# Optimization experiments

Hardware: AMD Instinct MI355X
Metric: run time of the kernel (lower is better)

Reference implementation:

```python
import jax, jax.numpy as jnp
import numpy as np

B, U, N, D, O = 64, 8, 2048, 512, 512  # batch, units, neurons, input_dim, output_dim
RES_CONN, IN_CONN, BIAS_P = 0.2, 0.2, 0.5


def setup_inputs() -> dict:
    key = jax.random.key(0)
    ks = jax.random.split(key, 10)
    # Recurrent weights: normal * sparse mask, normalized by ~spectral radius
    Wd = jax.random.normal(ks[0], (U, N, N), dtype=jnp.float32)
    Wmask = (jax.random.uniform(ks[1], (U, N, N)) < RES_CONN).astype(jnp.float32)
    W = Wd * Wmask / jnp.sqrt(RES_CONN * N)  # approx unit spectral radius
    # Input weights: fixed_bernoulli -> {0,1} sparse matrix
    Win = (jax.random.uniform(ks[2], (U, D, N)) < IN_CONN).astype(jnp.float32)
    bias = (jax.random.uniform(ks[3], (U, 1, N)) < BIAS_P).astype(jnp.float32)
    Wout = jax.random.normal(ks[4], (U, N, O), dtype=jnp.float32)
    sr = jax.random.uniform(ks[5], (U, 1, 1), dtype=jnp.float32)
    adaptive_lr = jax.random.uniform(ks[6], (U, D, 1), dtype=jnp.float32)
    temperature = jnp.ones((1,), dtype=jnp.float32)
    X = jax.random.normal(ks[7], (B, U, D), dtype=jnp.float32)
    state = jax.random.normal(ks[8], (B, U, N), dtype=jnp.float32)
    return {"X": X, "state": state, "W": W, "Win": Win, "bias": bias,
            "Wout": Wout, "sr": sr, "adaptive_lr": adaptive_lr,
            "temperature": temperature}


def reference(X, state, W, Win, bias, Wout, sr, adaptive_lr, temperature):
    # X: [B,U,D], state: [B,U,N]
    x = X[:, :, None, :]       # [B,U,1,D]
    s = state[:, :, None, :]   # [B,U,1,N]
    # adaptive learning rate: softmax over units
    logits = jnp.einsum('buid,udk->buik', x, adaptive_lr) / temperature  # [B,U,1,1]
    lr = jax.nn.softmax(logits, axis=1)
    # _sparse_mm_subhead == masked matmul (W's zeros contribute nothing)
    feed = jnp.einsum('bud,udn->bun', X, Win)[:, :, None, :]           # [B,U,1,N]
    echo = jnp.einsum('bun,unm->bum', state, W * sr)[:, :, None, :] + bias
    new_state = (1.0 - lr) * s + lr * jnp.tanh(feed + echo)            # [B,U,1,N]
    output = jnp.einsum('buin,uno->buio', new_state, Wout)             # [B,U,1,O]
    return new_state.squeeze(2), output.squeeze(2)
```

## Files before the change

### kernel.cpp

```cpp
#include <hip/hip_runtime.h>

#define B_ 64
#define U_ 8
#define N_ 2048
#define D_ 512
#define O_ 512
#define NS_ELEMS ((long)B_ * U_ * N_)

typedef __attribute__((ext_vector_type(8))) short short8;
typedef __attribute__((ext_vector_type(8))) float float8;
typedef __attribute__((ext_vector_type(4))) float float4v;
typedef __attribute__((ext_vector_type(4))) unsigned short ushort4v;
typedef __attribute__((ext_vector_type(16))) float floatx16;

__device__ __forceinline__ float bf2f(unsigned short b) {
    unsigned int u = ((unsigned int)b) << 16;
    float f; __builtin_memcpy(&f, &u, 4); return f;
}
__device__ __forceinline__ unsigned short f2bf(float f) {
    unsigned int u; __builtin_memcpy(&u, &f, 4);
    u += 0x7FFFu + ((u >> 16) & 1u);
    return (unsigned short)(u >> 16);
}
__device__ __forceinline__ bool is_bf(const void* temp) {
    return ((const unsigned short*)temp)[0] == 0x3F80u;
}
__device__ __forceinline__ float ldg1(const void* p, long i, bool bf) {
    return bf ? bf2f(((const unsigned short*)p)[i]) : ((const float*)p)[i];
}
__device__ __forceinline__ short8 ld8(const void* p, long i, bool bf) {
    if (bf) return *(const short8*)((const unsigned short*)p + i);
    float8 v = *(const float8*)((const float*)p + i);
    short8 r;
#pragma unroll
    for (int e = 0; e < 8; ++e) r[e] = (short)f2bf(v[e]);
    return r;
}
__device__ __forceinline__ short8 ld8s(const void* p, long i, bool bf, float s) {
    short8 r;
    if (bf) {
        short8 v = *(const short8*)((const unsigned short*)p + i);
#pragma unroll
        for (int e = 0; e < 8; ++e) r[e] = (short)f2bf(bf2f((unsigned short)v[e]) * s);
    } else {
        float8 v = *(const float8*)((const float*)p + i);
#pragma unroll
        for (int e = 0; e < 8; ++e) r[e] = (short)f2bf(v[e] * s);
    }
    return r;
}
__device__ __forceinline__ void stg1(void* p, long i, bool bf, float v) {
    if (bf) ((unsigned short*)p)[i] = f2bf(v); else ((float*)p)[i] = v;
}
__device__ __forceinline__ int swz(int row, int kbyte) {
    return row * 128 + (kbyte ^ ((row & 7) << 4));
}

__device__ __forceinline__ void gl_lds16(const void* g, void* l) {
    __builtin_amdgcn_global_load_lds(
        (const __attribute__((address_space(1))) unsigned int*)g,
        (__attribute__((address_space(3))) unsigned int*)l, 16, 0, 0);
}
#define WAITV(n) asm volatile("s_waitcnt vmcnt(" #n ")" ::: "memory")

template<bool BF, int NCH>
__device__ __forceinline__ void gemm_stream(
        const char* __restrict__ Apan, long arow_b,
        const char* __restrict__ Bpan, long brow_b,
        char* __restrict__ As,
        char* __restrict__ Bs,
        floatx16& acc, int t) {
    const int w = t >> 6, l = t & 63;
    const int mrow = (w >> 1) * 32 + (l & 31);
    const int ncol = (w & 1) * 32 + (l & 31);
    const int BCH = BF ? 8192 : 16384;
    const int a_r = w * 16 + (l >> 3);
    const long a_g = 16 * ((l & 7) ^ (l >> 3));

#define ISSUE(ck)                                                                   \
    {   char* Ad = As + ((ck) % 3) * 8192 + w * 2048;                               \
        const char* Ag0 = Apan + (long)(ck) * 128;                                  \
        gl_lds16(Ag0 + (long)a_r * arow_b + a_g, Ad);                               \
        gl_lds16(Ag0 + (long)(a_r + 8) * arow_b + a_g, Ad + 1024);                  \
        char* Bd = Bs + ((ck) % 3) * BCH;                                           \
        if (BF) {                                                                   \
            const char* Bg0 = Bpan +                                                \
                (long)((ck) * 64 + w * 16 + (l >> 3)) * brow_b + (l & 7) * 16;      \
            gl_lds16(Bg0, Bd + w * 2048);                                           \
            gl_lds16(Bg0 + 8 * brow_b, Bd + w * 2048 + 1024);                       \
        } else {                                                                    \
            const char* Bg0 = Bpan +                                                \
                (long)((ck) * 64 + w * 16 + (l >> 4)) * brow_b + (l & 15) * 16;     \
            gl_lds16(Bg0, Bd + w * 4096);                                           \
            gl_lds16(Bg0 + 4 * brow_b, Bd + w * 4096 + 1024);                       \
            gl_lds16(Bg0 + 8 * brow_b, Bd + w * 4096 + 2048);                       \
            gl_lds16(Bg0 + 12 * brow_b, Bd + w * 4096 + 3072);                      \
        } }

    ISSUE(0);
    ISSUE(1);
#pragma unroll
    for (int ck = 0; ck < NCH; ++ck) {
        if (ck + 2 < NCH) ISSUE(ck + 2);
        __builtin_amdgcn_sched_barrier(0);
        const int rem = NCH - 1 - ck;
        if (BF) { if (rem >= 2) WAITV(8); else if (rem == 1) WAITV(4); else WAITV(0); }
        else    { if (rem >= 2) WAITV(12); else if (rem == 1) WAITV(6); else WAITV(0); }
        __builtin_amdgcn_s_barrier();
        __builtin_amdgcn_sched_barrier(0);
        const char* Ac = As + (ck % 3) * 8192;
        const char* Bc = Bs + (ck % 3) * BCH;
#pragma unroll
        for (int ks = 0; ks < 4; ++ks) {
            int g = 2 * ks + (l >> 5);
            short8 a = *(const short8*)(Ac + swz(mrow, g * 16));
            short8 bfr;
            if (BF) {
#pragma unroll
                for (int e = 0; e < 8; ++e)
                    bfr[e] = *(const short*)(Bc + (g * 8 + e) * 128 + ncol * 2);
            } else {
#pragma unroll
                for (int e = 0; e < 8; ++e)
                    bfr[e] = (short)f2bf(*(const float*)(Bc + (g * 8 + e) * 256 + ncol * 4));
            }
            acc = __builtin_amdgcn_mfma_f32_32x32x16_bf16(a, bfr, acc, 0, 0, 0);
        }
        __builtin_amdgcn_sched_barrier(0);
        __builtin_amdgcn_s_barrier();
    }
#undef ISSUE
}

__global__ __launch_bounds__(256) void k0_pack(
        const void* __restrict__ state, const void* __restrict__ X,
        const void* __restrict__ sr, const void* __restrict__ temp,
        unsigned short* __restrict__ stC, unsigned short* __restrict__ xC) {
    const bool bf = is_bf(temp);
    const long i = ((long)blockIdx.x * 256 + threadIdx.x) * 4;
    ushort4v o;
    if (i < NS_ELEMS) {
        const int u = (int)(i >> 17), b = (int)((i >> 11) & 63), k = (int)(i & 2047);
        const float srv = ldg1(sr, u, bf);
#pragma unroll
        for (int e = 0; e < 4; ++e)
            o[e] = f2bf(ldg1(state, (long)(b * 8 + u) * 2048 + k + e, bf) * srv);
        *(ushort4v*)(stC + i) = o;
    } else {
        const long j = i - NS_ELEMS;
        const int u = (int)(j >> 15), b = (int)((j >> 9) & 63), k = (int)(j & 511);
#pragma unroll
        for (int e = 0; e < 4; ++e)
            o[e] = f2bf(ldg1(X, (long)(b * 8 + u) * 512 + k + e, bf));
        *(ushort4v*)(xC + j) = o;
    }
}

__global__ __launch_bounds__(512) void k1_lr(
        const void* __restrict__ X, const void* __restrict__ alr,
        const void* __restrict__ temp, float* __restrict__ lrbuf) {
    const bool bf = is_bf(temp);
    const int b = blockIdx.x;
    const int t = threadIdx.x;
    const int u = t >> 6, ln = t & 63;
    float s = 0.f;
#pragma unroll
    for (int e = 0; e < 8; ++e) {
        int d = ln * 8 + e;
        s += ldg1(X, (long)(b * 8 + u) * 512 + d, bf) * ldg1(alr, u * 512 + d, bf);
    }
#pragma unroll
    for (int off = 1; off < 64; off <<= 1) s += __shfl_xor(s, off);
    __shared__ float lg[U_];
    const float T = ldg1(temp, 0, bf);
    if (ln == 0) lg[u] = s / T;
    __syncthreads();
    if (t < U_) {
        float m = lg[0];
#pragma unroll
        for (int i = 1; i < U_; ++i) m = fmaxf(m, lg[i]);
        float den = 0.f;
#pragma unroll
        for (int i = 0; i < U_; ++i) den += expf(lg[i] - m);
        lrbuf[b * U_ + t] = expf(lg[t] - m) / den;
    }
}

template<bool BF>
__device__ __forceinline__ void k2s_body(
        const unsigned short* stC, const unsigned short* xC,
        const void* W, const void* Win, float* slabs,
        char* As, char* Bs, int bid, int t) {
    const int seg = bid >> 8;
    const int u   = (bid >> 5) & 7;
    const int n0  = (bid & 31) * 64;
    const int w = t >> 6, l = t & 63;
    const long esz = BF ? 2 : 4;
    floatx16 acc;
#pragma unroll
    for (int i = 0; i < 16; ++i) acc[i] = 0.f;

    if (seg == 0) {
        gemm_stream<BF, 8>((const char*)xC + (long)u * 65536, 1024,
                           (const char*)Win + ((long)u * D_ * N_ + n0) * esz, N_ * esz,
                           As, Bs, acc, t);
    } else {
        gemm_stream<BF, 8>((const char*)stC + (long)u * 262144 + (long)(seg - 1) * 1024, 4096,
                           (const char*)W + ((long)u * N_ * N_ + (long)(seg - 1) * 512 * N_ + n0) * esz,
                           N_ * esz, As, Bs, acc, t);
    }
    float* slab = slabs + (long)seg * NS_ELEMS;
    const int n = n0 + (w & 1) * 32 + (l & 31);
    const int rowbase = (w >> 1) * 32 + 4 * (l >> 5);
#pragma unroll
    for (int r = 0; r < 16; ++r) {
        int b = rowbase + (r & 3) + 8 * (r >> 2);
        slab[(long)b * (U_ * N_) + u * N_ + n] = acc[r];
    }
}

__global__ __launch_bounds__(256) void k2_stream(
        const unsigned short* __restrict__ stC, const unsigned short* __restrict__ xC,
        const void* __restrict__ W, const void* __restrict__ Win,
        const void* __restrict__ temp, float* __restrict__ slabs) {
    __shared__ alignas(16) char As[3 * 8192];
    __shared__ alignas(16) char Bs[3 * 16384];
    if (is_bf(temp))
        k2s_body<true >(stC, xC, W, Win, slabs, As, Bs, blockIdx.x, threadIdx.x);
    else
        k2s_body<false>(stC, xC, W, Win, slabs, As, Bs, blockIdx.x, threadIdx.x);
}

__global__ void k2b_mix(const float* __restrict__ slabs, const void* __restrict__ state,
                        const void* __restrict__ bias, const void* __restrict__ temp,
                        const float* __restrict__ lrbuf, void* __restrict__ ns,
                        unsigned short* __restrict__ nsC) {
    const bool bf = is_bf(temp);
    const long i = ((long)blockIdx.x * 256 + threadIdx.x) * 4;
    const int b = (int)(i >> 14);
    const int un = (int)(i & 16383);
    const int u = un >> 11, n = un & 2047;
    float4v s = *(const float4v*)(slabs + i);
#pragma unroll
    for (int seg = 1; seg < 5; ++seg) {
        float4v v = *(const float4v*)(slabs + (long)seg * NS_ELEMS + i);
#pragma unroll
        for (int e = 0; e < 4; ++e) s[e] += v[e];
    }
    const float lr = lrbuf[b * U_ + u];
    ushort4v oc;
#pragma unroll
    for (int e = 0; e < 4; ++e) {
        float st = ldg1(state, i + e, bf);
        float bv = ldg1(bias, u * N_ + n + e, bf);
        float v = (1.f - lr) * st + lr * tanhf(s[e] + bv);
        stg1(ns, i + e, bf, v);
        oc[e] = f2bf(v);
    }
    *(ushort4v*)(nsC + ((long)u * 64 + b) * 2048 + n) = oc;
}

template<bool BF>
__device__ __forceinline__ void k3s_body(
        const unsigned short* nsC, const void* Wout, float* part,
        char* As, char* Bs, int bid, int t) {
    const int kc = bid >> 6;
    const int u  = (bid >> 3) & 7;
    const int ot = bid & 7;
    const int o0 = ot * 64;
    const int w = t >> 6, l = t & 63;
    const long esz = BF ? 2 : 4;
    floatx16 acc;
#pragma unroll
    for (int i = 0; i < 16; ++i) acc[i] = 0.f;
    gemm_stream<BF, 4>((const char*)nsC + (long)u * 262144 + (long)kc * 512, 4096,
                       (const char*)Wout + ((long)u * N_ * O_ + (long)kc * 256 * O_ + o0) * esz,
                       O_ * esz, As, Bs, acc, t);
    float* slab = part + (((kc * 8 + u) * 8 + ot) << 12);
    const int oo = (w & 1) * 32 + (l & 31);
    const int rowbase = (w >> 1) * 32 + 4 * (l >> 5);
#pragma unroll
    for (int r = 0; r < 16; ++r) {
        int b = rowbase + (r & 3) + 8 * (r >> 2);
        slab[b * 64 + oo] = acc[r];
    }
}

__global__ __launch_bounds__(256) void k3_stream(
        const unsigned short* __restrict__ nsC, const void* __restrict__ Wout,
        const void* __restrict__ temp, float* __restrict__ part) {
    __shared__ alignas(16) char As[3 * 8192];
    __shared__ alignas(16) char Bs[3 * 16384];
    if (is_bf(temp))
        k3s_body<true >(nsC, Wout, part, As, Bs, blockIdx.x, threadIdx.x);
    else
        k3s_body<false>(nsC, Wout, part, As, Bs, blockIdx.x, threadIdx.x);
}

__global__ void k3_reduce(const float* __restrict__ part, const void* __restrict__ temp,
                          void* __restrict__ outfull, int kcs) {
    const bool bf = is_bf(temp);
    int i = blockIdx.x * 256 + threadIdx.x;
    int b = i >> 12;
    int u = (i >> 9) & 7;
    int o = i & 511;
    int ot = o >> 6, oo = o & 63;
    float s = 0.f;
    for (int kc = 0; kc < kcs; ++kc)
        s += part[(((kc * 8 + u) * 8 + ot) << 12) + b * 64 + oo];
    stg1(outfull, NS_ELEMS + i, bf, s);
}

__global__ __launch_bounds__(256) void k2_state(
        const void* __restrict__ X, const void* __restrict__ state,
        const void* __restrict__ W, const void* __restrict__ Win,
        const void* __restrict__ bias, const void* __restrict__ sr,
        const void* __restrict__ temp, const float* __restrict__ lrbuf,
        void* __restrict__ ns) {
    const bool bf = is_bf(temp);
    const int u  = blockIdx.x >> 5;
    const int n0 = (blockIdx.x & 31) * 64;
    const int t = threadIdx.x;
    const int w = t >> 6, l = t & 63;
    __shared__ alignas(16) char As[8192];
    __shared__ alignas(16) char Bs[8192];
    const float srv = ldg1(sr, u, bf);
    floatx16 acc;
#pragma unroll
    for (int i = 0; i < 16; ++i) acc[i] = 0.f;
    for (int ck = 0; ck < 40; ++ck) {
        const bool feed = ck < 8;
        const void* Ag; long aoff; int lda; float ascale;
        const void* Bg; long boff;
        if (feed) {
            Ag = X;   aoff = (long)u * D_ + ck * 64;          lda = U_ * D_; ascale = 1.f;
            Bg = Win; boff = (long)u * D_ * N_ + (long)(ck * 64) * N_ + n0;
        } else {
            Ag = state; aoff = (long)u * N_ + (ck - 8) * 64;  lda = U_ * N_; ascale = srv;
            Bg = W;     boff = (long)u * N_ * N_ + (long)((ck - 8) * 64) * N_ + n0;
        }
        __syncthreads();
#pragma unroll
        for (int j = 0; j < 2; ++j) {
            int idx = j * 256 + t;
            int row = idx >> 3, cch = idx & 7;
            short8 v = ld8s(Ag, aoff + (long)row * lda + cch * 8, bf, ascale);
            *(short8*)(As + swz(row, cch * 16)) = v;
        }
#pragma unroll
        for (int j = 0; j < 2; ++j) {
            int k = t & 63;
            int c = (t >> 6) + 4 * j;
            short8 v = ld8(Bg, boff + (long)k * N_ + c * 8, bf);
#pragma unroll
            for (int e = 0; e < 8; ++e) {
                int n = c * 8 + e;
                *(unsigned short*)(Bs + swz(n, 2 * k)) = (unsigned short)v[e];
            }
        }
        __syncthreads();
        const int mrow = (w >> 1) * 32 + (l & 31);
        const int ncol = (w & 1) * 32 + (l & 31);
#pragma unroll
        for (int ks = 0; ks < 4; ++ks) {
            int g = 2 * ks + (l >> 5);
            short8 a = *(const short8*)(As + swz(mrow, g * 16));
            short8 b = *(const short8*)(Bs + swz(ncol, g * 16));
            acc = __builtin_amdgcn_mfma_f32_32x32x16_bf16(a, b, acc, 0, 0, 0);
        }
    }
    const int n = n0 + (w & 1) * 32 + (l & 31);
    const int rowbase = (w >> 1) * 32 + 4 * (l >> 5);
    const float biasv = ldg1(bias, u * N_ + n, bf);
#pragma unroll
    for (int r = 0; r < 16; ++r) {
        int b = rowbase + (r & 3) + 8 * (r >> 2);
        float lr = lrbuf[b * U_ + u];
        float st = ldg1(state, (long)b * U_ * N_ + u * N_ + n, bf);
        float v = (1.f - lr) * st + lr * tanhf(acc[r] + biasv);
        stg1(ns, (long)b * U_ * N_ + u * N_ + n, bf, v);
    }
}

__global__ __launch_bounds__(256) void k3_mono(
        const void* __restrict__ ns, const void* __restrict__ Wout,
        const void* __restrict__ temp, void* __restrict__ outfull) {
    const bool bf = is_bf(temp);
    const int u  = (blockIdx.x >> 3) & 7;
    const int ot = blockIdx.x & 7;
    const int o0 = ot * 64;
    const int t = threadIdx.x;
    const int w = t >> 6, l = t & 63;
    __shared__ alignas(16) char As[8192];
    __shared__ alignas(16) char Bs[8192];
    floatx16 acc;
#pragma unroll
    for (int i = 0; i < 16; ++i) acc[i] = 0.f;
    for (int ck = 0; ck < 32; ++ck) {
        const long ka = (long)(ck * 64);
        __syncthreads();
#pragma unroll
        for (int j = 0; j < 2; ++j) {
            int idx = j * 256 + t;
            int row = idx >> 3, cch = idx & 7;
            short8 v = ld8(ns, (long)row * (U_ * N_) + u * N_ + ka + cch * 8, bf);
            *(short8*)(As + swz(row, cch * 16)) = v;
        }
#pragma unroll
        for (int j = 0; j < 2; ++j) {
            int k = t & 63;
            int c = (t >> 6) + 4 * j;
            short8 v = ld8(Wout, (long)u * N_ * O_ + (ka + k) * O_ + o0 + c * 8, bf);
#pragma unroll
            for (int e = 0; e < 8; ++e) {
                int n = c * 8 + e;
                *(unsigned short*)(Bs + swz(n, 2 * k)) = (unsigned short)v[e];
            }
        }
        __syncthreads();
        const int mrow = (w >> 1) * 32 + (l & 31);
        const int ncol = (w & 1) * 32 + (l & 31);
#pragma unroll
        for (int ks = 0; ks < 4; ++ks) {
            int g = 2 * ks + (l >> 5);
            short8 a = *(const short8*)(As + swz(mrow, g * 16));
            short8 b = *(const short8*)(Bs + swz(ncol, g * 16));
            acc = __builtin_amdgcn_mfma_f32_32x32x16_bf16(a, b, acc, 0, 0, 0);
        }
    }
    const int oo = (w & 1) * 32 + (l & 31);
    const int rowbase = (w >> 1) * 32 + 4 * (l >> 5);
#pragma unroll
    for (int r = 0; r < 16; ++r) {
        int b = rowbase + (r & 3) + 8 * (r >> 2);
        stg1(outfull, NS_ELEMS + (long)b * U_ * O_ + u * O_ + o0 + oo, bf, acc[r]);
    }
}

extern "C" void kernel_launch(void* const* d_in, const int* in_sizes, int n_in,
                              void* d_out, int out_size, void* d_ws, size_t ws_size,
                              hipStream_t stream) {
    const void* X     = d_in[0];
    const void* state = d_in[1];
    const void* W     = d_in[2];
    const void* Win   = d_in[3];
    const void* bias  = d_in[4];
    const void* Wout  = d_in[5];
    const void* sr    = d_in[6];
    const void* alr   = d_in[7];
    const void* temp  = d_in[8];

    char* base = (char*)d_ws;
    float* lrbuf        = (float*)base;
    unsigned short* stC = (unsigned short*)(base + 4096);
    unsigned short* xC  = (unsigned short*)(base + 4096 + (2u << 20));
    unsigned short* nsC = (unsigned short*)(base + 4096 + (2u << 20) + (512u << 10));
    float* slabs        = (float*)(base + (8u << 20));
    const size_t need = (8u << 20) + 5 * (size_t)NS_ELEMS * 4;

    k1_lr<<<B_, 512, 0, stream>>>(X, alr, temp, lrbuf);

    if (ws_size >= need) {
        k0_pack  <<<1280, 256, 0, stream>>>(state, X, sr, temp, stC, xC);
        k2_stream<<<1280, 256, 0, stream>>>(stC, xC, W, Win, temp, slabs);
        k2b_mix  <<<NS_ELEMS / 1024, 256, 0, stream>>>(slabs, state, bias, temp, lrbuf, d_out, nsC);
        k3_stream<<<512, 256, 0, stream>>>(nsC, Wout, temp, slabs);
        k3_reduce<<<(B_ * U_ * O_) / 256, 256, 0, stream>>>(slabs, temp, d_out, 8);
    } else {
        k2_state<<<256, 256, 0, stream>>>(X, state, W, Win, bias, sr, temp, lrbuf, d_out);
        k3_mono <<<64, 256, 0, stream>>>(d_out, Wout, temp, d_out);
    }
}
```

Baseline: 70.47 us.

## Rebalance split-K into 3 bf16 slabs and remap block order per XCD

```diff
diff --git a/kernel.cpp b/kernel.cpp
--- a/kernel.cpp
+++ b/kernel.cpp
@@ -6,6 +6,7 @@
 #define D_ 512
 #define O_ 512
 #define NS_ELEMS ((long)B_ * U_ * N_)
+#define OUT_ELEMS ((long)B_ * U_ * O_)
 
 typedef __attribute__((ext_vector_type(8))) short short8;
 typedef __attribute__((ext_vector_type(8))) float float8;
@@ -189,7 +190,7 @@
 template<bool BF>
 __device__ __forceinline__ void k2s_body(
         const unsigned short* stC, const unsigned short* xC,
-        const void* W, const void* Win, float* slabs,
+        const void* W, const void* Win, unsigned short* slabs,
         char* As, char* Bs, int bid, int t) {
     const int seg = bid >> 8;
     const int u   = (bid >> 5) & 7;
@@ -200,38 +201,46 @@
 #pragma unroll
     for (int i = 0; i < 16; ++i) acc[i] = 0.f;
 
+    const char* stP = (const char*)stC + (long)u * 262144;
+    const char* Wp  = (const char*)W + ((long)u * N_ * N_ + n0) * esz;
+
     if (seg == 0) {
         gemm_stream<BF, 8>((const char*)xC + (long)u * 65536, 1024,
                            (const char*)Win + ((long)u * D_ * N_ + n0) * esz, N_ * esz,
                            As, Bs, acc, t);
+        gemm_stream<BF, 8>(stP, 4096, Wp, N_ * esz, As, Bs, acc, t);
+    } else if (seg == 1) {
+        gemm_stream<BF, 12>(stP + 1024, 4096, Wp + (long)512 * N_ * esz, N_ * esz,
+                            As, Bs, acc, t);
     } else {
-        gemm_stream<BF, 8>((const char*)stC + (long)u * 262144 + (long)(seg - 1) * 1024, 4096,
-                           (const char*)W + ((long)u * N_ * N_ + (long)(seg - 1) * 512 * N_ + n0) * esz,
-                           N_ * esz, As, Bs, acc, t);
-    }
-    float* slab = slabs + (long)seg * NS_ELEMS;
+        gemm_stream<BF, 12>(stP + 2560, 4096, Wp + (long)1280 * N_ * esz, N_ * esz,
+                            As, Bs, acc, t);
+    }
+    unsigned short* slab = slabs + (long)seg * NS_ELEMS;
     const int n = n0 + (w & 1) * 32 + (l & 31);
     const int rowbase = (w >> 1) * 32 + 4 * (l >> 5);
 #pragma unroll
     for (int r = 0; r < 16; ++r) {
         int b = rowbase + (r & 3) + 8 * (r >> 2);
-        slab[(long)b * (U_ * N_) + u * N_ + n] = acc[r];
+        slab[(long)b * (U_ * N_) + u * N_ + n] = f2bf(acc[r]);
     }
 }
 
 __global__ __launch_bounds__(256) void k2_stream(
         const unsigned short* __restrict__ stC, const unsigned short* __restrict__ xC,
         const void* __restrict__ W, const void* __restrict__ Win,
-        const void* __restrict__ temp, float* __restrict__ slabs) {
+        const void* __restrict__ temp, unsigned short* __restrict__ slabs) {
     __shared__ alignas(16) char As[3 * 8192];
     __shared__ alignas(16) char Bs[3 * 16384];
+    const int bid = (blockIdx.x % 8) * 96 + blockIdx.x / 8;
     if (is_bf(temp))
-        k2s_body<true >(stC, xC, W, Win, slabs, As, Bs, blockIdx.x, threadIdx.x);
+        k2s_body<true >(stC, xC, W, Win, slabs, As, Bs, bid, threadIdx.x);
     else
-        k2s_body<false>(stC, xC, W, Win, slabs, As, Bs, blockIdx.x, threadIdx.x);
-}
-
-__global__ void k2b_mix(const float* __restrict__ slabs, const void* __restrict__ state,
+        k2s_body<false>(stC, xC, W, Win, slabs, As, Bs, bid, threadIdx.x);
+}
+
+__global__ void k2b_mix(const unsigned short* __restrict__ slabs,
+                        const void* __restrict__ state,
                         const void* __restrict__ bias, const void* __restrict__ temp,
                         const float* __restrict__ lrbuf, void* __restrict__ ns,
                         unsigned short* __restrict__ nsC) {
@@ -240,12 +249,13 @@
     const int b = (int)(i >> 14);
     const int un = (int)(i & 16383);
     const int u = un >> 11, n = un & 2047;
-    float4v s = *(const float4v*)(slabs + i);
-#pragma unroll
-    for (int seg = 1; seg < 5; ++seg) {
-        float4v v = *(const float4v*)(slabs + (long)seg * NS_ELEMS + i);
-#pragma unroll
-        for (int e = 0; e < 4; ++e) s[e] += v[e];
+    float4v s;
+    {
+        ushort4v v0 = *(const ushort4v*)(slabs + i);
+        ushort4v v1 = *(const ushort4v*)(slabs + NS_ELEMS + i);
+        ushort4v v2 = *(const ushort4v*)(slabs + 2 * NS_ELEMS + i);
+#pragma unroll
+        for (int e = 0; e < 4; ++e) s[e] = bf2f(v0[e]) + bf2f(v1[e]) + bf2f(v2[e]);
     }
     const float lr = lrbuf[b * U_ + u];
     ushort4v oc;
@@ -262,7 +272,7 @@
 
 template<bool BF>
 __device__ __forceinline__ void k3s_body(
-        const unsigned short* nsC, const void* Wout, float* part,
+        const unsigned short* nsC, const void* Wout, unsigned short* part,
         char* As, char* Bs, int bid, int t) {
     const int kc = bid >> 6;
     const int u  = (bid >> 3) & 7;
@@ -276,29 +286,31 @@
     gemm_stream<BF, 4>((const char*)nsC + (long)u * 262144 + (long)kc * 512, 4096,
                        (const char*)Wout + ((long)u * N_ * O_ + (long)kc * 256 * O_ + o0) * esz,
                        O_ * esz, As, Bs, acc, t);
-    float* slab = part + (((kc * 8 + u) * 8 + ot) << 12);
+    unsigned short* slab = part + (((kc * 8 + u) * 8 + ot) << 12);
     const int oo = (w & 1) * 32 + (l & 31);
     const int rowbase = (w >> 1) * 32 + 4 * (l >> 5);
 #pragma unroll
     for (int r = 0; r < 16; ++r) {
         int b = rowbase + (r & 3) + 8 * (r >> 2);
-        slab[b * 64 + oo] = acc[r];
+        slab[b * 64 + oo] = f2bf(acc[r]);
     }
 }
 
 __global__ __launch_bounds__(256) void k3_stream(
         const unsigned short* __restrict__ nsC, const void* __restrict__ Wout,
-        const void* __restrict__ temp, float* __restrict__ part) {
+        const void* __restrict__ temp, unsigned short* __restrict__ part) {
     __shared__ alignas(16) char As[3 * 8192];
     __shared__ alignas(16) char Bs[3 * 16384];
+    const int bid = (blockIdx.x % 8) * 64 + blockIdx.x / 8;
     if (is_bf(temp))
-        k3s_body<true >(nsC, Wout, part, As, Bs, blockIdx.x, threadIdx.x);
+        k3s_body<true >(nsC, Wout, part, As, Bs, bid, threadIdx.x);
     else
-        k3s_body<false>(nsC, Wout, part, As, Bs, blockIdx.x, threadIdx.x);
-}
-
-__global__ void k3_reduce(const float* __restrict__ part, const void* __restrict__ temp,
-                          void* __restrict__ outfull, int kcs) {
+        k3s_body<false>(nsC, Wout, part, As, Bs, bid, threadIdx.x);
+}
+
+__global__ void k3_reduce(const unsigned short* __restrict__ part,
+                          const void* __restrict__ temp,
+                          void* __restrict__ outfull) {
     const bool bf = is_bf(temp);
     int i = blockIdx.x * 256 + threadIdx.x;
     int b = i >> 12;
@@ -306,8 +318,9 @@
     int o = i & 511;
     int ot = o >> 6, oo = o & 63;
     float s = 0.f;
-    for (int kc = 0; kc < kcs; ++kc)
-        s += part[(((kc * 8 + u) * 8 + ot) << 12) + b * 64 + oo];
+#pragma unroll
+    for (int kc = 0; kc < 8; ++kc)
+        s += bf2f(part[(((kc * 8 + u) * 8 + ot) << 12) + b * 64 + oo]);
     stg1(outfull, NS_ELEMS + i, bf, s);
 }
 
@@ -455,17 +468,17 @@
     unsigned short* stC = (unsigned short*)(base + 4096);
     unsigned short* xC  = (unsigned short*)(base + 4096 + (2u << 20));
     unsigned short* nsC = (unsigned short*)(base + 4096 + (2u << 20) + (512u << 10));
-    float* slabs        = (float*)(base + (8u << 20));
-    const size_t need = (8u << 20) + 5 * (size_t)NS_ELEMS * 4;
+    unsigned short* slabs = (unsigned short*)(base + (8u << 20));
+    const size_t need = (8u << 20) + 3 * (size_t)NS_ELEMS * 2;
 
     k1_lr<<<B_, 512, 0, stream>>>(X, alr, temp, lrbuf);
 
     if (ws_size >= need) {
         k0_pack  <<<1280, 256, 0, stream>>>(state, X, sr, temp, stC, xC);
-        k2_stream<<<1280, 256, 0, stream>>>(stC, xC, W, Win, temp, slabs);
+        k2_stream<<<768, 256, 0, stream>>>(stC, xC, W, Win, temp, slabs);
         k2b_mix  <<<NS_ELEMS / 1024, 256, 0, stream>>>(slabs, state, bias, temp, lrbuf, d_out, nsC);
         k3_stream<<<512, 256, 0, stream>>>(nsC, Wout, temp, slabs);
-        k3_reduce<<<(B_ * U_ * O_) / 256, 256, 0, stream>>>(slabs, temp, d_out, 8);
+        k3_reduce<<<OUT_ELEMS / 256, 256, 0, stream>>>(slabs, temp, d_out);
     } else {
         k2_state<<<256, 256, 0, stream>>>(X, state, W, Win, bias, sr, temp, lrbuf, d_out);
         k3_mono <<<64, 256, 0, stream>>>(d_out, Wout, temp, d_out);
```

New measurement: 66.99 us. 4.9% less time.
